# Kernel optimization log

Measured on AMD Instinct MI355X. Metric: run time of the kernel, lower is better.

The kernel has to match this reference:

```python
import jax, jax.numpy as jnp
from jax import lax
import numpy as np

S = 2048      # seq_len
E = 1024      # embedding_dim
H = 512       # hidden per direction (hidden_dim // 2)
V = 50000     # vocab
T = 16        # tagset_size
START, STOP = 0, 1
NEG = -10000.0


def setup_inputs() -> dict:
    key = jax.random.key(0)
    ks = jax.random.split(key, 20)
    bound = 1.0 / np.sqrt(H)

    def u(k, shape):
        return jax.random.uniform(k, shape, minval=-bound, maxval=bound, dtype=jnp.float32)

    sentence = jax.random.randint(ks[0], (S,), 0, V)
    emb = jax.random.normal(ks[1], (V, E), dtype=jnp.float32) * 0.1
    # PyTorch LSTM weights, gate order (i, f, g, o) stacked along first dim
    Wih_f = u(ks[2], (4 * H, E)); Whh_f = u(ks[3], (4 * H, H))
    bih_f = u(ks[4], (4 * H,));   bhh_f = u(ks[5], (4 * H,))
    Wih_b = u(ks[6], (4 * H, E)); Whh_b = u(ks[7], (4 * H, H))
    bih_b = u(ks[8], (4 * H,));   bhh_b = u(ks[9], (4 * H,))
    # init_hidden(): randn initial (h0, c0), [2 directions, H] (batch=1 squeezed)
    h0 = jax.random.normal(ks[10], (2, H), dtype=jnp.float32)
    c0 = jax.random.normal(ks[11], (2, H), dtype=jnp.float32)
    Wout = u(ks[12], (T, 2 * H)); bout = u(ks[13], (T,))
    transitions = jax.random.normal(ks[14], (T, T), dtype=jnp.float32)
    transitions = transitions.at[START, :].set(NEG).at[:, STOP].set(NEG)
    return dict(sentence=sentence, emb=emb,
                Wih_f=Wih_f, Whh_f=Whh_f, bih_f=bih_f, bhh_f=bhh_f,
                Wih_b=Wih_b, Whh_b=Whh_b, bih_b=bih_b, bhh_b=bhh_b,
                h0=h0, c0=c0, Wout=Wout, bout=bout, transitions=transitions)


def _lstm_dir(x, Wih, Whh, bih, bhh, h0, c0):
    # x: [S, E] -> hs: [S, H]; PyTorch gate order i, f, g, o
    xg = x @ Wih.T + bih + bhh  # precompute input contribution [S, 4H]

    def step(carry, xg_t):
        h, c = carry
        g = xg_t + h @ Whh.T
        i, f, gg, o = jnp.split(g, 4)
        i, f, o = jax.nn.sigmoid(i), jax.nn.sigmoid(f), jax.nn.sigmoid(o)
        c = f * c + i * jnp.tanh(gg)
        h = o * jnp.tanh(c)
        return (h, c), h

    _, hs = lax.scan(step, (h0, c0), xg)
    return hs


def _feats(sentence, emb, Wih_f, Whh_f, bih_f, bhh_f, Wih_b, Whh_b, bih_b, bhh_b,
           h0, c0, Wout, bout):
    x = emb[sentence]  # [S, E]
    hf = _lstm_dir(x, Wih_f, Whh_f, bih_f, bhh_f, h0[0], c0[0])              # [S, H]
    hb = _lstm_dir(x[::-1], Wih_b, Whh_b, bih_b, bhh_b, h0[1], c0[1])[::-1]  # [S, H]
    out = jnp.concatenate([hf, hb], axis=-1)  # [S, 2H]
    return out @ Wout.T + bout                # [S, T]


def _viterbi(feats, transitions):
    v0 = jnp.full((T,), NEG, dtype=feats.dtype).at[START].set(0.0)

    def vstep(v, feat):
        scores = v[None, :] + transitions        # [T(next), T(prev)]
        bp = jnp.argmax(scores, axis=1)          # best prev tag per next tag
        v_new = jnp.max(scores, axis=1) + feat
        return v_new, bp

    v, bps = lax.scan(vstep, v0, feats)          # bps: [S, T]
    terminal = v + transitions[STOP]
    best = jnp.argmax(terminal)
    path_score = terminal[best]

    def btstep(tag, bp):
        return bp[tag], tag

    _, path = lax.scan(btstep, best, bps, reverse=True)  # path[t] = tag at t
    return path_score, path


def reference(sentence, emb, Wih_f, Whh_f, bih_f, bhh_f, Wih_b, Whh_b, bih_b, bhh_b,
              h0, c0, Wout, bout, transitions):
    feats = _feats(sentence, emb, Wih_f, Whh_f, bih_f, bhh_f,
                   Wih_b, Whh_b, bih_b, bhh_b, h0, c0, Wout, bout)
    path_score, path = _viterbi(feats, transitions)
    return path_score, path
```

## Files before the change

kernel.cpp:

```cpp
#include <hip/hip_runtime.h>
#include <hip/hip_bf16.h>

#define S 2048
#define NEGV -10000.0f

typedef unsigned long long ull;
typedef unsigned int uint4v __attribute__((ext_vector_type(4)));

__device__ __forceinline__ float fsig(float x) {
  return 1.0f / (1.0f + __expf(-x));
}
__device__ __forceinline__ float ftanh(float x) {
  float a = fabsf(x);
  float e = __expf(-2.0f * a);
  float r = (1.0f - e) / (1.0f + e);
  return copysignf(r, x);
}

__global__ void init_h_k(const float* __restrict__ h0, ull* __restrict__ hbuf) {
  int dir = blockIdx.x;
  int u = threadIdx.x;
  ull pk = (1ULL << 32) | (ull)__float_as_uint(h0[dir * 512 + u]);
  __hip_atomic_store(&hbuf[dir * 1024 + u], pk, __ATOMIC_RELAXED, __HIP_MEMORY_SCOPE_AGENT);
  __hip_atomic_store(&hbuf[dir * 1024 + 512 + u], 0ULL, __ATOMIC_RELAXED, __HIP_MEMORY_SCOPE_AGENT);
}

__global__ __launch_bounds__(256) void gemm_xg_k(
    const int* __restrict__ sent, const float* __restrict__ emb,
    const float* __restrict__ Wih_f, const float* __restrict__ Wih_b,
    const float* __restrict__ bih_f, const float* __restrict__ bhh_f,
    const float* __restrict__ bih_b, const float* __restrict__ bhh_b,
    float* __restrict__ xg)
{
  __shared__ __align__(16) float Asm[64 * 36];
  __shared__ __align__(16) float Bsm[32 * 68];
  __shared__ int sidx[64];

  const int bx = blockIdx.x;
  const int by = blockIdx.y;
  const int t = threadIdx.x;
  const int n0 = bx * 64, m0 = by * 64;

  const float* W = (n0 < 2048) ? (Wih_f + (size_t)n0 * 1024)
                               : (Wih_b + (size_t)(n0 - 2048) * 1024);
  if (t < 64) sidx[t] = sent[m0 + t];
  __syncthreads();

  const int tm = t >> 4, tn = t & 15;
  const int lr = t >> 2, lkq = t & 3;
  float acc[4][4] = {};

  for (int k0 = 0; k0 < 1024; k0 += 32) {
    const float* ap = emb + (size_t)sidx[lr] * 1024 + k0 + lkq * 8;
    float4 a0 = *(const float4*)ap;
    float4 a1 = *(const float4*)(ap + 4);
    const float* bp = W + (size_t)lr * 1024 + k0 + lkq * 8;
    float4 b0 = *(const float4*)bp;
    float4 b1 = *(const float4*)(bp + 4);
    __syncthreads();
    *(float4*)&Asm[lr * 36 + lkq * 8]     = a0;
    *(float4*)&Asm[lr * 36 + lkq * 8 + 4] = a1;
    {
      const float* bb0 = (const float*)&b0;
      const float* bb1 = (const float*)&b1;
      #pragma unroll
      for (int j = 0; j < 4; ++j) Bsm[(lkq * 8 + j) * 68 + lr] = bb0[j];
      #pragma unroll
      for (int j = 0; j < 4; ++j) Bsm[(lkq * 8 + 4 + j) * 68 + lr] = bb1[j];
    }
    __syncthreads();
    #pragma unroll
    for (int kk = 0; kk < 32; ++kk) {
      float a0_ = Asm[(tm * 4 + 0) * 36 + kk];
      float a1_ = Asm[(tm * 4 + 1) * 36 + kk];
      float a2_ = Asm[(tm * 4 + 2) * 36 + kk];
      float a3_ = Asm[(tm * 4 + 3) * 36 + kk];
      float4 bv = *(const float4*)&Bsm[kk * 68 + tn * 4];
      acc[0][0] = fmaf(a0_, bv.x, acc[0][0]); acc[0][1] = fmaf(a0_, bv.y, acc[0][1]);
      acc[0][2] = fmaf(a0_, bv.z, acc[0][2]); acc[0][3] = fmaf(a0_, bv.w, acc[0][3]);
      acc[1][0] = fmaf(a1_, bv.x, acc[1][0]); acc[1][1] = fmaf(a1_, bv.y, acc[1][1]);
      acc[1][2] = fmaf(a1_, bv.z, acc[1][2]); acc[1][3] = fmaf(a1_, bv.w, acc[1][3]);
      acc[2][0] = fmaf(a2_, bv.x, acc[2][0]); acc[2][1] = fmaf(a2_, bv.y, acc[2][1]);
      acc[2][2] = fmaf(a2_, bv.z, acc[2][2]); acc[2][3] = fmaf(a2_, bv.w, acc[2][3]);
      acc[3][0] = fmaf(a3_, bv.x, acc[3][0]); acc[3][1] = fmaf(a3_, bv.y, acc[3][1]);
      acc[3][2] = fmaf(a3_, bv.z, acc[3][2]); acc[3][3] = fmaf(a3_, bv.w, acc[3][3]);
    }
  }

  const float* bi = (n0 < 2048) ? bih_f : bih_b;
  const float* bh = (n0 < 2048) ? bhh_f : bhh_b;
  const int nb = (n0 < 2048) ? n0 : (n0 - 2048);
  #pragma unroll
  for (int i = 0; i < 4; ++i) {
    int m = m0 + tm * 4 + i;
    #pragma unroll
    for (int j = 0; j < 4; ++j) {
      int nn = tn * 4 + j;
      float bias = bi[nb + nn] + bh[nb + nn];
      xg[(size_t)m * 4096 + n0 + nn] = acc[i][j] + bias;
    }
  }
}

__global__ __launch_bounds__(256, 1) void lstm_rec_k(
    const float* __restrict__ Whh_f, const float* __restrict__ Whh_b,
    const float* __restrict__ c0,
    const float* __restrict__ xg,
    ull* __restrict__ hbuf,
    float* __restrict__ hs_cat)
{
  const int w = blockIdx.x;
  const int dir = w & 1;
  const int wid = w >> 1;
  const int t = threadIdx.x;
  const int rr = t >> 3;
  const int seg = t & 7;
  const int g  = rr & 3;
  const int ul = rr >> 2;
  const int unit = wid * 8 + ul;
  const int grow = g * 512 + unit;

  const float* Whh = dir ? Whh_b : Whh_f;

  float wreg[64];
  {
    const float* src = Whh + (size_t)grow * 512 + seg * 64;
    #pragma unroll
    for (int j = 0; j < 16; ++j) {
      float4 v = *(const float4*)(src + j * 4);
      wreg[4 * j + 0] = v.x; wreg[4 * j + 1] = v.y;
      wreg[4 * j + 2] = v.z; wreg[4 * j + 3] = v.w;
    }
  }

  __shared__ __align__(16) float h_lds[2][544];

  ull* hb = hbuf + dir * 1024;

  float c_reg = c0[dir * 512 + unit];

  const int u0 = t * 2;
  const int wchunk = u0 >> 6;
  const int wpos   = u0 & 63;

  float xg_a = 0.0f, xg_b = 0.0f;
  if (seg == 0) {
    int r0 = dir ? (S - 1) : 0;
    int r1 = dir ? (S - 2) : 1;
    xg_a = xg[(size_t)r0 * 4096 + dir * 2048 + grow];
    xg_b = xg[(size_t)r1 * 4096 + dir * 2048 + grow];
  }

  #define LSTM_STEP(K, XG_REG)                                                  \
  {                                                                             \
    const int k = (K);                                                          \
    float xgv = XG_REG;                                                         \
    if (seg == 0 && k + 2 < S) {                \
      int rowk = dir ? (S - 3 - k) : (k + 2);                                   \
      XG_REG = xg[(size_t)rowk * 4096 + dir * 2048 + grow];                     \
    }                                                                           \
         \
    {                                                                           \
      ull* src = hb + (k & 1) * 512 + u0;                                       \
      const unsigned want = (unsigned)(k + 1);                                  \
      uint4v v;                                                                 \
      asm volatile("global_load_dwordx4 %0, %1, off sc0 sc1"                    \
                   : "=v"(v) : "v"(src) : "memory");                            \
      asm volatile("s_waitcnt vmcnt(0)" ::: "memory");                          \
      while (v.y != want || v.w != want) {                                      \
        __builtin_amdgcn_s_sleep(2);                                            \
        asm volatile("global_load_dwordx4 %0, %1, off sc0 sc1"                  \
                     : "=v"(v) : "v"(src) : "memory");                          \
        asm volatile("s_waitcnt vmcnt(0)" ::: "memory");                        \
      }                                                                         \
      float* dst = &h_lds[k & 1][wchunk * 68 + wpos];                           \
      dst[0] = __uint_as_float(v.x);                                            \
      dst[1] = __uint_as_float(v.z);                                            \
    }                                                                           \
    __syncthreads();                                                            \
                                         \
    const float* hl = &h_lds[k & 1][0];                                         \
    float p0 = 0.f, p1 = 0.f, p2 = 0.f, p3 = 0.f;                               \
    const float4* h4 = (const float4*)(hl + seg * 68);                          \
    _Pragma("unroll")                                                           \
    for (int j = 0; j < 16; ++j) {                                              \
      float4 hv = h4[j];                                                        \
      p0 = fmaf(wreg[4 * j + 0], hv.x, p0);                                     \
      p1 = fmaf(wreg[4 * j + 1], hv.y, p1);                                     \
      p2 = fmaf(wreg[4 * j + 2], hv.z, p2);                                     \
      p3 = fmaf(wreg[4 * j + 3], hv.w, p3);                                     \
    }                                                                           \
    float p = (p0 + p1) + (p2 + p3) + xgv;                                      \
    p += __shfl_xor(p, 1);                                                      \
    p += __shfl_xor(p, 2);                                                      \
    p += __shfl_xor(p, 4);                                                      \
    float gb_ = __shfl_xor(p, 8);                                 \
    float gc_ = __shfl_xor(p, 16);                                \
    float gd_ = __shfl_xor(gb_, 16);                              \
    if (g == 0) {                                                               \
      float iv = fsig(p), fv = fsig(gb_), ov = fsig(gd_);                       \
      float gv = ftanh(gc_);                                                    \
      c_reg = fv * c_reg + iv * gv;                                             \
      float hv = ov * ftanh(c_reg);                                             \
      if (seg == 0) {                                                           \
        ull pk = ((ull)(unsigned)(k + 2) << 32) | (ull)__float_as_uint(hv);     \
        __hip_atomic_store(&hb[((k + 1) & 1) * 512 + unit], pk,                 \
                           __ATOMIC_RELAXED, __HIP_MEMORY_SCOPE_AGENT);         \
        int orig = dir ? (S - 1 - k) : k;                                       \
        hs_cat[(size_t)orig * 1024 + dir * 512 + unit] = hv;                    \
      }                                                                         \
    }                                                                           \
  }

  for (int kk = 0; kk < S; kk += 2) {
    LSTM_STEP(kk, xg_a);
    LSTM_STEP(kk + 1, xg_b);
  }
  #undef LSTM_STEP
}

__global__ __launch_bounds__(64) void feats_k(
    const float* __restrict__ hs_cat, const float* __restrict__ Wout,
    const float* __restrict__ bout, float* __restrict__ feats)
{
  int tpos = blockIdx.x;
  int l = threadIdx.x;
  int j = l & 15, q = l >> 4;
  const float* h = hs_cat + (size_t)tpos * 1024 + q * 256;
  const float* wv = Wout + (size_t)j * 1024 + q * 256;
  float s = 0.f;
  #pragma unroll 8
  for (int i = 0; i < 256; i += 4) {
    float4 hv = *(const float4*)(h + i);
    float4 ww = *(const float4*)(wv + i);
    s = fmaf(hv.x, ww.x, s); s = fmaf(hv.y, ww.y, s);
    s = fmaf(hv.z, ww.z, s); s = fmaf(hv.w, ww.w, s);
  }
  s += __shfl_xor(s, 16);
  s += __shfl_xor(s, 32);
  if (q == 0) feats[tpos * 16 + j] = s + bout[j];
}

__global__ __launch_bounds__(64, 1) void viterbi_k(
    const float* __restrict__ feats, const float* __restrict__ trans,
    float* __restrict__ out)
{
  __shared__ __align__(16) float fch[2][256 * 16];
  __shared__ unsigned char bp4[S * 8];
  __shared__ float v_lds[2][16];

  const int l = threadIdx.x;
  const int next = l & 15, q = l >> 4;

  float tr0 = trans[next * 16 + q * 4 + 0];
  float tr1 = trans[next * 16 + q * 4 + 1];
  float tr2 = trans[next * 16 + q * 4 + 2];
  float tr3 = trans[next * 16 + q * 4 + 3];

  if (l < 16) v_lds[0][l] = (l == 0) ? 0.0f : NEGV;

  const float4* f4 = (const float4*)feats;
  float4 buf[16];
  #pragma unroll
  for (int i = 0; i < 16; ++i) buf[i] = f4[i * 64 + l];
  #pragma unroll
  for (int i = 0; i < 16; ++i) ((float4*)fch[0])[i * 64 + l] = buf[i];
  __syncthreads();

  for (int c = 0; c < 8; ++c) {
    if (c < 7) {
      #pragma unroll
      for (int i = 0; i < 16; ++i) buf[i] = f4[(c + 1) * 1024 + i * 64 + l];
    }
    const float* fc = fch[c & 1];
    for (int tt = 0; tt < 256; ++tt) {
      int t = c * 256 + tt;
      int pb = t & 1;
      const float* vin = v_lds[pb];
      float m = vin[q * 4 + 0] + tr0; int mi = q * 4;
      float s1 = vin[q * 4 + 1] + tr1; if (s1 > m) { m = s1; mi = q * 4 + 1; }
      float s2 = vin[q * 4 + 2] + tr2; if (s2 > m) { m = s2; mi = q * 4 + 2; }
      float s3 = vin[q * 4 + 3] + tr3; if (s3 > m) { m = s3; mi = q * 4 + 3; }
      #pragma unroll
      for (int mask = 16; mask <= 32; mask <<= 1) {
        float om = __shfl_xor(m, mask);
        int omi = __shfl_xor(mi, mask);
        if (om > m || (om == m && omi < mi)) { m = om; mi = omi; }
      }
      int pmi = __shfl_xor(mi, 1);
      if (q == 0) {
        v_lds[pb ^ 1][next] = m + fc[tt * 16 + next];
        if ((next & 1) == 0)
          bp4[t * 8 + (next >> 1)] = (unsigned char)((mi & 15) | ((pmi & 15) << 4));
      }
      __syncthreads();
    }
    if (c < 7) {
      #pragma unroll
      for (int i = 0; i < 16; ++i) ((float4*)fch[(c + 1) & 1])[i * 64 + l] = buf[i];
      __syncthreads();
    }
  }

  float term = (l < 16) ? (v_lds[0][l] + trans[1 * 16 + l]) : -3.0e38f;
  int ti = (l < 16) ? l : 0;
  #pragma unroll
  for (int mask = 1; mask <= 32; mask <<= 1) {
    float om = __shfl_xor(term, mask);
    int omi = __shfl_xor(ti, mask);
    if (om > term || (om == term && omi < ti)) { term = om; ti = omi; }
  }
  if (l == 0) {
    out[0] = term;
    int tag = ti;
    out[1 + (S - 1)] = (float)tag;
    for (int t = S - 1; t >= 1; --t) {
      tag = (bp4[t * 8 + (tag >> 1)] >> ((tag & 1) * 4)) & 15;
      out[t] = (float)tag;
    }
  }
}

extern "C" void kernel_launch(void* const* d_in, const int* in_sizes, int n_in,
                              void* d_out, int out_size, void* d_ws, size_t ws_size,
                              hipStream_t stream) {
  const int*   sent  = (const int*)d_in[0];
  const float* emb   = (const float*)d_in[1];
  const float* Wih_f = (const float*)d_in[2];
  const float* Whh_f = (const float*)d_in[3];
  const float* bih_f = (const float*)d_in[4];
  const float* bhh_f = (const float*)d_in[5];
  const float* Wih_b = (const float*)d_in[6];
  const float* Whh_b = (const float*)d_in[7];
  const float* bih_b = (const float*)d_in[8];
  const float* bhh_b = (const float*)d_in[9];
  const float* h0    = (const float*)d_in[10];
  const float* c0    = (const float*)d_in[11];
  const float* Wout  = (const float*)d_in[12];
  const float* bout  = (const float*)d_in[13];
  const float* trans = (const float*)d_in[14];
  float* out = (float*)d_out;

  char* ws = (char*)d_ws;
  float* xg     = (float*)(ws);
  float* hs_cat = (float*)(ws + 33554432);
  float* feats  = (float*)(ws + 41943040);
  ull*   hbuf   = (ull*)  (ws + 42074112);

  init_h_k<<<2, 512, 0, stream>>>(h0, hbuf);
  gemm_xg_k<<<dim3(64, 32), 256, 0, stream>>>(sent, emb, Wih_f, Wih_b,
                                              bih_f, bhh_f, bih_b, bhh_b, xg);
  lstm_rec_k<<<128, 256, 0, stream>>>(Whh_f, Whh_b, c0, xg, hbuf, hs_cat);
  feats_k<<<2048, 64, 0, stream>>>(hs_cat, Wout, bout, feats);
  viterbi_k<<<1, 64, 0, stream>>>(feats, trans, out);
}
```

Measured before the change: 4.034 ms.

## Fuse input-projection GEMM with LSTM recurrence using per-tile ready flags

Merges the xg GEMM and the recurrent LSTM kernel into one persistent launch. Blocks 128-255 compute GEMM tiles in an order that follows the sequence front of each direction, then publish a per-tile flag. Recurrent blocks spin on the flag before reading each new 64-row slab of xg. The aim is to hide the GEMM behind the serial recurrence instead of running it first. This relies on all 256 blocks being co-resident, and the GEMM blocks now compete with the recurrence for bandwidth. The h-poll sleep interval is also shortened.

```diff
diff --git a/kernel.cpp b/kernel.cpp
--- a/kernel.cpp
+++ b/kernel.cpp
@@ -15,6 +15,10 @@
   float e = __expf(-2.0f * a);
   float r = (1.0f - e) / (1.0f + e);
   return copysignf(r, x);
+}
+
+__global__ void clear_flags_k(int* __restrict__ flags) {
+  flags[blockIdx.x * 256 + threadIdx.x] = 0;
 }
 
 __global__ void init_h_k(const float* __restrict__ h0, ull* __restrict__ hbuf) {
@@ -25,103 +29,115 @@
   __hip_atomic_store(&hbuf[dir * 1024 + 512 + u], 0ULL, __ATOMIC_RELAXED, __HIP_MEMORY_SCOPE_AGENT);
 }
 
-__global__ __launch_bounds__(256) void gemm_xg_k(
+__global__ __launch_bounds__(256) void fused_k(
     const int* __restrict__ sent, const float* __restrict__ emb,
     const float* __restrict__ Wih_f, const float* __restrict__ Wih_b,
     const float* __restrict__ bih_f, const float* __restrict__ bhh_f,
     const float* __restrict__ bih_b, const float* __restrict__ bhh_b,
-    float* __restrict__ xg)
-{
-  __shared__ __align__(16) float Asm[64 * 36];
-  __shared__ __align__(16) float Bsm[32 * 68];
-  __shared__ int sidx[64];
-
-  const int bx = blockIdx.x;
-  const int by = blockIdx.y;
-  const int t = threadIdx.x;
-  const int n0 = bx * 64, m0 = by * 64;
-
-  const float* W = (n0 < 2048) ? (Wih_f + (size_t)n0 * 1024)
-                               : (Wih_b + (size_t)(n0 - 2048) * 1024);
-  if (t < 64) sidx[t] = sent[m0 + t];
-  __syncthreads();
-
-  const int tm = t >> 4, tn = t & 15;
-  const int lr = t >> 2, lkq = t & 3;
-  float acc[4][4] = {};
-
-  for (int k0 = 0; k0 < 1024; k0 += 32) {
-    const float* ap = emb + (size_t)sidx[lr] * 1024 + k0 + lkq * 8;
-    float4 a0 = *(const float4*)ap;
-    float4 a1 = *(const float4*)(ap + 4);
-    const float* bp = W + (size_t)lr * 1024 + k0 + lkq * 8;
-    float4 b0 = *(const float4*)bp;
-    float4 b1 = *(const float4*)(bp + 4);
-    __syncthreads();
-    *(float4*)&Asm[lr * 36 + lkq * 8]     = a0;
-    *(float4*)&Asm[lr * 36 + lkq * 8 + 4] = a1;
-    {
-      const float* bb0 = (const float*)&b0;
-      const float* bb1 = (const float*)&b1;
-      #pragma unroll
-      for (int j = 0; j < 4; ++j) Bsm[(lkq * 8 + j) * 68 + lr] = bb0[j];
-      #pragma unroll
-      for (int j = 0; j < 4; ++j) Bsm[(lkq * 8 + 4 + j) * 68 + lr] = bb1[j];
-    }
-    __syncthreads();
-    #pragma unroll
-    for (int kk = 0; kk < 32; ++kk) {
-      float a0_ = Asm[(tm * 4 + 0) * 36 + kk];
-      float a1_ = Asm[(tm * 4 + 1) * 36 + kk];
-      float a2_ = Asm[(tm * 4 + 2) * 36 + kk];
-      float a3_ = Asm[(tm * 4 + 3) * 36 + kk];
-      float4 bv = *(const float4*)&Bsm[kk * 68 + tn * 4];
-      acc[0][0] = fmaf(a0_, bv.x, acc[0][0]); acc[0][1] = fmaf(a0_, bv.y, acc[0][1]);
-      acc[0][2] = fmaf(a0_, bv.z, acc[0][2]); acc[0][3] = fmaf(a0_, bv.w, acc[0][3]);
-      acc[1][0] = fmaf(a1_, bv.x, acc[1][0]); acc[1][1] = fmaf(a1_, bv.y, acc[1][1]);
-      acc[1][2] = fmaf(a1_, bv.z, acc[1][2]); acc[1][3] = fmaf(a1_, bv.w, acc[1][3]);
-      acc[2][0] = fmaf(a2_, bv.x, acc[2][0]); acc[2][1] = fmaf(a2_, bv.y, acc[2][1]);
-      acc[2][2] = fmaf(a2_, bv.z, acc[2][2]); acc[2][3] = fmaf(a2_, bv.w, acc[2][3]);
-      acc[3][0] = fmaf(a3_, bv.x, acc[3][0]); acc[3][1] = fmaf(a3_, bv.y, acc[3][1]);
-      acc[3][2] = fmaf(a3_, bv.z, acc[3][2]); acc[3][3] = fmaf(a3_, bv.w, acc[3][3]);
-    }
-  }
-
-  const float* bi = (n0 < 2048) ? bih_f : bih_b;
-  const float* bh = (n0 < 2048) ? bhh_f : bhh_b;
-  const int nb = (n0 < 2048) ? n0 : (n0 - 2048);
-  #pragma unroll
-  for (int i = 0; i < 4; ++i) {
-    int m = m0 + tm * 4 + i;
-    #pragma unroll
-    for (int j = 0; j < 4; ++j) {
-      int nn = tn * 4 + j;
-      float bias = bi[nb + nn] + bh[nb + nn];
-      xg[(size_t)m * 4096 + n0 + nn] = acc[i][j] + bias;
-    }
-  }
-}
-
-__global__ __launch_bounds__(256, 1) void lstm_rec_k(
     const float* __restrict__ Whh_f, const float* __restrict__ Whh_b,
     const float* __restrict__ c0,
-    const float* __restrict__ xg,
+    float* __restrict__ xg,
     ull* __restrict__ hbuf,
-    float* __restrict__ hs_cat)
+    float* __restrict__ hs_cat,
+    int* __restrict__ flags)
 {
+  __shared__ __align__(16) float smem[4544];
+  const int t = threadIdx.x;
+
+  if (blockIdx.x >= 128) {
+    float* Asm = smem;
+    float* Bsm = smem + 2304;
+    int*   sidx = (int*)(smem + 4480);
+    const int tm = t >> 4, tn = t & 15;
+    const int lr = t >> 2, lkq = t & 3;
+
+    for (int i = 0; i < 16; ++i) {
+      const int T = (blockIdx.x - 128) + 128 * i;
+      const int byo = T >> 6, bxo = T & 63;
+      const int by = (byo & 1) ? (31 - (byo >> 1)) : (byo >> 1);
+      const int bx = (bxo & 1) ? (32 + (bxo >> 1)) : (bxo >> 1);
+      const int n0 = bx * 64, m0 = by * 64;
+
+      const float* W = (n0 < 2048) ? (Wih_f + (size_t)n0 * 1024)
+                                   : (Wih_b + (size_t)(n0 - 2048) * 1024);
+      __syncthreads();
+      if (t < 64) sidx[t] = sent[m0 + t];
+      __syncthreads();
+
+      float acc[4][4] = {};
+      for (int k0 = 0; k0 < 1024; k0 += 32) {
+        const float* ap = emb + (size_t)sidx[lr] * 1024 + k0 + lkq * 8;
+        float4 a0 = *(const float4*)ap;
+        float4 a1 = *(const float4*)(ap + 4);
+        const float* bp = W + (size_t)lr * 1024 + k0 + lkq * 8;
+        float4 b0 = *(const float4*)bp;
+        float4 b1 = *(const float4*)(bp + 4);
+        __syncthreads();
+        *(float4*)&Asm[lr * 36 + lkq * 8]     = a0;
+        *(float4*)&Asm[lr * 36 + lkq * 8 + 4] = a1;
+        {
+          const float* bb0 = (const float*)&b0;
+          const float* bb1 = (const float*)&b1;
+          #pragma unroll
+          for (int j = 0; j < 4; ++j) Bsm[(lkq * 8 + j) * 68 + lr] = bb0[j];
+          #pragma unroll
+          for (int j = 0; j < 4; ++j) Bsm[(lkq * 8 + 4 + j) * 68 + lr] = bb1[j];
+        }
+        __syncthreads();
+        #pragma unroll
+        for (int kk = 0; kk < 32; ++kk) {
+          float a0_ = Asm[(tm * 4 + 0) * 36 + kk];
+          float a1_ = Asm[(tm * 4 + 1) * 36 + kk];
+          float a2_ = Asm[(tm * 4 + 2) * 36 + kk];
+          float a3_ = Asm[(tm * 4 + 3) * 36 + kk];
+          float4 bv = *(const float4*)&Bsm[kk * 68 + tn * 4];
+          acc[0][0] = fmaf(a0_, bv.x, acc[0][0]); acc[0][1] = fmaf(a0_, bv.y, acc[0][1]);
+          acc[0][2] = fmaf(a0_, bv.z, acc[0][2]); acc[0][3] = fmaf(a0_, bv.w, acc[0][3]);
+          acc[1][0] = fmaf(a1_, bv.x, acc[1][0]); acc[1][1] = fmaf(a1_, bv.y, acc[1][1]);
+          acc[1][2] = fmaf(a1_, bv.z, acc[1][2]); acc[1][3] = fmaf(a1_, bv.w, acc[1][3]);
+          acc[2][0] = fmaf(a2_, bv.x, acc[2][0]); acc[2][1] = fmaf(a2_, bv.y, acc[2][1]);
+          acc[2][2] = fmaf(a2_, bv.z, acc[2][2]); acc[2][3] = fmaf(a2_, bv.w, acc[2][3]);
+          acc[3][0] = fmaf(a3_, bv.x, acc[3][0]); acc[3][1] = fmaf(a3_, bv.y, acc[3][1]);
+          acc[3][2] = fmaf(a3_, bv.z, acc[3][2]); acc[3][3] = fmaf(a3_, bv.w, acc[3][3]);
+        }
+      }
+
+      const float* bi = (n0 < 2048) ? bih_f : bih_b;
+      const float* bh = (n0 < 2048) ? bhh_f : bhh_b;
+      const int nb = (n0 < 2048) ? n0 : (n0 - 2048);
+      #pragma unroll
+      for (int ii = 0; ii < 4; ++ii) {
+        int m = m0 + tm * 4 + ii;
+        #pragma unroll
+        for (int j = 0; j < 4; ++j) {
+          int nn = tn * 4 + j;
+          float bias = bi[nb + nn] + bh[nb + nn];
+          __hip_atomic_store(&xg[(size_t)m * 4096 + n0 + nn], acc[ii][j] + bias,
+                             __ATOMIC_RELAXED, __HIP_MEMORY_SCOPE_AGENT);
+        }
+      }
+      asm volatile("s_waitcnt vmcnt(0)" ::: "memory");
+      __syncthreads();
+      if (t == 0)
+        __hip_atomic_store(&flags[by * 64 + bx], 1, __ATOMIC_RELAXED, __HIP_MEMORY_SCOPE_AGENT);
+    }
+    return;
+  }
+
   const int w = blockIdx.x;
   const int dir = w & 1;
   const int wid = w >> 1;
-  const int t = threadIdx.x;
   const int rr = t >> 3;
   const int seg = t & 7;
   const int g  = rr & 3;
   const int ul = rr >> 2;
   const int unit = wid * 8 + ul;
   const int grow = g * 512 + unit;
+  const int bxf  = dir * 32 + g * 8 + (wid >> 3);
+
+  float (*h_lds)[544] = (float(*)[544])smem;
 
   const float* Whh = dir ? Whh_b : Whh_f;
-
   float wreg[64];
   {
     const float* src = Whh + (size_t)grow * 512 + seg * 64;
@@ -133,31 +149,40 @@
     }
   }
 
-  __shared__ __align__(16) float h_lds[2][544];
-
   ull* hb = hbuf + dir * 1024;
-
   float c_reg = c0[dir * 512 + unit];
 
   const int u0 = t * 2;
-  const int wchunk = u0 >> 6;
-  const int wpos   = u0 & 63;
+  const int wchunk = u0 >> 6, wpos = u0 & 63;
 
   float xg_a = 0.0f, xg_b = 0.0f;
   if (seg == 0) {
+    int by0 = dir ? 31 : 0;
+    while (__hip_atomic_load(&flags[by0 * 64 + bxf], __ATOMIC_RELAXED,
+                             __HIP_MEMORY_SCOPE_AGENT) != 1)
+      __builtin_amdgcn_s_sleep(8);
     int r0 = dir ? (S - 1) : 0;
     int r1 = dir ? (S - 2) : 1;
-    xg_a = xg[(size_t)r0 * 4096 + dir * 2048 + grow];
-    xg_b = xg[(size_t)r1 * 4096 + dir * 2048 + grow];
+    xg_a = __hip_atomic_load(&xg[(size_t)r0 * 4096 + dir * 2048 + grow],
+                             __ATOMIC_RELAXED, __HIP_MEMORY_SCOPE_AGENT);
+    xg_b = __hip_atomic_load(&xg[(size_t)r1 * 4096 + dir * 2048 + grow],
+                             __ATOMIC_RELAXED, __HIP_MEMORY_SCOPE_AGENT);
   }
 
   #define LSTM_STEP(K, XG_REG)                                                  \
   {                                                                             \
     const int k = (K);                                                          \
     float xgv = XG_REG;                                                         \
-    if (seg == 0 && k + 2 < S) {                \
+    if (seg == 0 && k + 2 < S) {            \
       int rowk = dir ? (S - 3 - k) : (k + 2);                                   \
-      XG_REG = xg[(size_t)rowk * 4096 + dir * 2048 + grow];                     \
+      if ((rowk & 63) == (dir ? 63 : 0)) {       \
+        int byn = rowk >> 6;                                                    \
+        while (__hip_atomic_load(&flags[byn * 64 + bxf], __ATOMIC_RELAXED,      \
+                                 __HIP_MEMORY_SCOPE_AGENT) != 1)                \
+          __builtin_amdgcn_s_sleep(8);                                          \
+      }                                                                         \
+      XG_REG = __hip_atomic_load(&xg[(size_t)rowk * 4096 + dir * 2048 + grow],  \
+                                 __ATOMIC_RELAXED, __HIP_MEMORY_SCOPE_AGENT);   \
     }                                                                           \
          \
     {                                                                           \
@@ -168,7 +193,7 @@
                    : "=v"(v) : "v"(src) : "memory");                            \
       asm volatile("s_waitcnt vmcnt(0)" ::: "memory");                          \
       while (v.y != want || v.w != want) {                                      \
-        __builtin_amdgcn_s_sleep(2);                                            \
+        __builtin_amdgcn_s_sleep(1);                                            \
         asm volatile("global_load_dwordx4 %0, %1, off sc0 sc1"                  \
                      : "=v"(v) : "v"(src) : "memory");                          \
         asm volatile("s_waitcnt vmcnt(0)" ::: "memory");                        \
@@ -346,11 +371,13 @@
   float* hs_cat = (float*)(ws + 33554432);
   float* feats  = (float*)(ws + 41943040);
   ull*   hbuf   = (ull*)  (ws + 42074112);
-
+  int*   flags  = (int*)  (ws + 42090496);
+
+  clear_flags_k<<<8, 256, 0, stream>>>(flags);
   init_h_k<<<2, 512, 0, stream>>>(h0, hbuf);
-  gemm_xg_k<<<dim3(64, 32), 256, 0, stream>>>(sent, emb, Wih_f, Wih_b,
-                                              bih_f, bhh_f, bih_b, bhh_b, xg);
-  lstm_rec_k<<<128, 256, 0, stream>>>(Whh_f, Whh_b, c0, xg, hbuf, hs_cat);
+  fused_k<<<256, 256, 0, stream>>>(sent, emb, Wih_f, Wih_b, bih_f, bhh_f,
+                                   bih_b, bhh_b, Whh_f, Whh_b, c0,
+                                   xg, hbuf, hs_cat, flags);
   feats_k<<<2048, 64, 0, stream>>>(hs_cat, Wout, bout, feats);
   viterbi_k<<<1, 64, 0, stream>>>(feats, trans, out);
 }
```

After: 3.921 ms. 2.8% less time.
